# Performance work log

Hardware: AMD Instinct MI355X
Metric: run time of the kernel (lower is better)

Reference implementation:

```python
import jax, jax.numpy as jnp
import numpy as np

B, S, D_IN, D, H, HD, HALF, L = 64, 500, 64, 128, 8, 16, 5, 2
WIN = 2 * HALF + 1  # 11 attended positions per query
EPS = 1e-12  # HF layer_norm_eps default


def _ln(x, g, b):
    m = x.mean(-1, keepdims=True)
    v = ((x - m) ** 2).mean(-1, keepdims=True)
    return (x - m) / jnp.sqrt(v + EPS) * g + b


def setup_inputs() -> dict:
    key = jax.random.key(0)
    ks = jax.random.split(key, 24)
    n = lambda i, shape: jax.random.normal(ks[i], shape, jnp.float32) * 0.02
    return {
        "x": jax.random.normal(ks[0], (B, S, D_IN), jnp.float32),
        "W_in": n(1, (D_IN, D)), "b_in": jnp.zeros((D,), jnp.float32),
        "pos_emb": n(2, (512, D)), "tt_emb": n(3, (D,)),
        "ln_emb_g": jnp.ones((D,), jnp.float32), "ln_emb_b": jnp.zeros((D,), jnp.float32),
        "Wq": n(4, (L, D, D)), "bq": jnp.zeros((L, D), jnp.float32),
        "Wk": n(5, (L, D, D)), "bk": jnp.zeros((L, D), jnp.float32),
        "Wv": n(6, (L, D, D)), "bv": jnp.zeros((L, D), jnp.float32),
        "Wo": n(7, (L, D, D)), "bo": jnp.zeros((L, D), jnp.float32),
        "ln1_g": jnp.ones((L, D), jnp.float32), "ln1_b": jnp.zeros((L, D), jnp.float32),
        "Wi": n(8, (L, D, 512)), "bi": jnp.zeros((L, 512), jnp.float32),
        "Wo2": n(9, (L, 512, D)), "bo2": jnp.zeros((L, D), jnp.float32),
        "ln2_g": jnp.ones((L, D), jnp.float32), "ln2_b": jnp.zeros((L, D), jnp.float32),
        "W_cls": n(10, (D, 2)), "b_cls": jnp.zeros((2,), jnp.float32),
    }


def reference(x, W_in, b_in, pos_emb, tt_emb, ln_emb_g, ln_emb_b,
              Wq, bq, Wk, bk, Wv, bv, Wo, bo, ln1_g, ln1_b,
              Wi, bi, Wo2, bo2, ln2_g, ln2_b, W_cls, b_cls):
    # input projection + RoBERTa-style embeddings (position ids start at padding_idx+1=2)
    h = x @ W_in + b_in
    pos_ids = 2 + jnp.arange(S)
    h = _ln(h + pos_emb[pos_ids] + tt_emb, ln_emb_g, ln_emb_b)

    # sliding-window gather indices: each query attends [i-HALF, i+HALF]
    idx = jnp.arange(S)[:, None] + jnp.arange(-HALF, HALF + 1)[None, :]
    valid = (idx >= 0) & (idx < S)
    idxc = jnp.clip(idx, 0, S - 1)
    scale = 1.0 / jnp.sqrt(jnp.float32(HD))

    for l in range(L):
        qh = (h @ Wq[l] + bq[l]).reshape(B, S, H, HD).transpose(0, 2, 1, 3)
        kh = (h @ Wk[l] + bk[l]).reshape(B, S, H, HD).transpose(0, 2, 1, 3)
        vh = (h @ Wv[l] + bv[l]).reshape(B, S, H, HD).transpose(0, 2, 1, 3)
        kk = kh[:, :, idxc]
        scores = jnp.einsum('bhsd,bhswd->bhsw', qh * scale, kk)
        scores = jnp.where(valid, scores, -jnp.inf)
        probs = jax.nn.softmax(scores, axis=-1)
        vv = vh[:, :, idxc]
        ctx = jnp.einsum('bhsw,bhswd->bhsd', probs, vv)
        ctx = ctx.transpose(0, 2, 1, 3).reshape(B, S, D)
        h = _ln(ctx @ Wo[l] + bo[l] + h, ln1_g[l], ln1_b[l])
        ff = jax.nn.gelu(h @ Wi[l] + bi[l], approximate=False) @ Wo2[l] + bo2[l]
        h = _ln(ff + h, ln2_g[l], ln2_b[l])

    pooled = h.mean(axis=1)  # mean over sequence
    return pooled @ W_cls + b_cls
```

## Files before the change

### kernel.cpp

```cpp
#include <hip/hip_runtime.h>
#include <hip/hip_bf16.h>
#include <math.h>

#define BB 64
#define SS 500
#define DIN 64
#define DD 128
#define HH 8
#define HDIM 16
#define HALF_ 5
#define WINW 11
#define LL 2
#define FF 512
#define MM (BB*SS)
#define LN_EPS 1e-12f

typedef __attribute__((ext_vector_type(8))) short short8;
typedef __attribute__((ext_vector_type(4))) float f32x4;

__global__ __launch_bounds__(256) void k_prep(
    const float* __restrict__ Wq, const float* __restrict__ Wk,
    const float* __restrict__ Wv, const float* __restrict__ Wo,
    const float* __restrict__ Wi, const float* __restrict__ Wo2,
    __hip_bfloat16* __restrict__ wT)
{
    const int m = blockIdx.y;
    const int l = m / 6, t = m % 6;
    const float* src; int Kd, Nd, kshift, doff;
    switch (t) {
      case 0:  src = Wq  + l*16384; Kd=128; Nd=128; kshift=7; doff=0;      break;
      case 1:  src = Wk  + l*16384; Kd=128; Nd=128; kshift=7; doff=16384;  break;
      case 2:  src = Wv  + l*16384; Kd=128; Nd=128; kshift=7; doff=32768;  break;
      case 3:  src = Wo  + l*16384; Kd=128; Nd=128; kshift=7; doff=49152;  break;
      case 4:  src = Wi  + l*65536; Kd=128; Nd=512; kshift=7; doff=65536;  break;
      default: src = Wo2 + l*65536; Kd=512; Nd=128; kshift=9; doff=131072; break;
    }
    __hip_bfloat16* dst = wT + l*196608 + doff;
    const int NK = Kd * Nd;
    int e = (blockIdx.x * 256 + threadIdx.x) * 4;
    if (e >= NK) return;
    #pragma unroll
    for (int j = 0; j < 4; ++j, ++e) {
        int n = e >> kshift, kx = e & (Kd - 1);
        dst[(size_t)n * Kd + kx] = __float2bfloat16(src[(size_t)kx * Nd + n]);
    }
}

__global__ __launch_bounds__(256) void k_embed(
    const float* __restrict__ x, const float* __restrict__ Win,
    const float* __restrict__ bin, const float* __restrict__ pos,
    const float* __restrict__ tt, const float* __restrict__ g,
    const float* __restrict__ be, float* __restrict__ h,
    __hip_bfloat16* __restrict__ hbf)
{
    __shared__ float WinS[DIN][DD];
    __shared__ float xs[16][DIN];
    __shared__ float rs[4][2];

    const int tid = threadIdx.x;
    const int d    = tid & 127;
    const int rp   = tid >> 7;
    const int wid  = tid >> 6;
    const int row0 = blockIdx.x * 16;

    #pragma unroll
    for (int it = 0; it < 8; ++it) {
        int lin = it * 1024 + tid * 4;
        *(float4*)&WinS[lin >> 7][lin & 127] = *(const float4*)(Win + lin);
    }
    {
        int lin = tid * 4;
        *(float4*)&xs[lin >> 6][lin & 63] =
            *(const float4*)(x + (size_t)row0 * DIN + lin);
    }
    __syncthreads();

    const float bd = bin[d] + tt[d];

    for (int it = 0; it < 8; ++it) {
        const int r   = it * 2 + rp;
        const int row = row0 + r;
        const int s   = row % SS;

        float acc = bd + pos[(size_t)(2 + s) * DD + d];
        #pragma unroll 8
        for (int i = 0; i < DIN; ++i) acc += xs[r][i] * WinS[i][d];

        float s1 = acc, s2 = acc * acc;
        #pragma unroll
        for (int off = 1; off < 64; off <<= 1) {
            s1 += __shfl_xor(s1, off);
            s2 += __shfl_xor(s2, off);
        }
        if ((tid & 63) == 0) { rs[wid][0] = s1; rs[wid][1] = s2; }
        __syncthreads();
        const float S1 = rs[rp * 2][0] + rs[rp * 2 + 1][0];
        const float S2 = rs[rp * 2][1] + rs[rp * 2 + 1][1];
        const float mean = S1 * (1.0f / DD);
        const float var  = S2 * (1.0f / DD) - mean * mean;
        const float rstd = rsqrtf(var + LN_EPS);
        const float o = (acc - mean) * rstd * g[d] + be[d];
        h[(size_t)row * DD + d]   = o;
        hbf[(size_t)row * DD + d] = __float2bfloat16(o);
        __syncthreads();
    }
}

#define GEMM_MAIN(Abf, lda, Kdim, WTbf, ldw, n0w)                             \
    __shared__ __align__(16) __hip_bfloat16 As[128][72];                      \
    __shared__ __align__(16) __hip_bfloat16 Ws[128][72];                      \
    const int tid = threadIdx.x;                                              \
    const int wid = tid >> 6;                                                 \
    const int l15 = tid & 15;                                                 \
    const int l4  = (tid & 63) >> 4;                                          \
    const int m0  = blockIdx.x * 128;                                         \
    f32x4 acc[2][8];                                                          \
    _Pragma("unroll")                                                         \
    for (int m = 0; m < 2; ++m)                                               \
        _Pragma("unroll")                                                     \
        for (int n = 0; n < 8; ++n) acc[m][n] = (f32x4){0.f, 0.f, 0.f, 0.f};  \
    for (int k0 = 0; k0 < (Kdim); k0 += 64) {                                 \
        _Pragma("unroll")                                                     \
        for (int it = 0; it < 4; ++it) {                                      \
            int lin = it * 2048 + tid * 8;                                    \
            int r = lin >> 6, c = lin & 63;                                   \
            *(uint4*)&As[r][c] =                                              \
                *(const uint4*)((Abf) + (size_t)(m0 + r) * (lda) + k0 + c);   \
            *(uint4*)&Ws[r][c] =                                              \
                *(const uint4*)((WTbf) + (size_t)((n0w) + r) * (ldw) + k0 + c); \
        }                                                                     \
        __syncthreads();                                                      \
        for (int kc = 0; kc < 64; kc += 32) {                                 \
            short8 a0 = *(const short8*)&As[wid * 32 +      l15][kc + l4 * 8];\
            short8 a1 = *(const short8*)&As[wid * 32 + 16 + l15][kc + l4 * 8];\
            _Pragma("unroll")                                                 \
            for (int n = 0; n < 8; ++n) {                                     \
                short8 bf = *(const short8*)&Ws[n * 16 + l15][kc + l4 * 8];   \
                acc[0][n] = __builtin_amdgcn_mfma_f32_16x16x32_bf16(a0, bf, acc[0][n], 0, 0, 0); \
                acc[1][n] = __builtin_amdgcn_mfma_f32_16x16x32_bf16(a1, bf, acc[1][n], 0, 0, 0); \
            }                                                                 \
        }                                                                     \
        __syncthreads();                                                      \
    }

__global__ __launch_bounds__(256, 4) void k_gemm_qkv(
    const __hip_bfloat16* __restrict__ hbf,
    const __hip_bfloat16* __restrict__ wTq, const __hip_bfloat16* __restrict__ wTk,
    const __hip_bfloat16* __restrict__ wTv,
    const float* __restrict__ bq, const float* __restrict__ bk,
    const float* __restrict__ bv,
    float* __restrict__ q, float* __restrict__ k, float* __restrict__ v)
{
    const __hip_bfloat16* WT; const float* bias; float* out;
    if (blockIdx.y == 0)      { WT = wTq; bias = bq; out = q; }
    else if (blockIdx.y == 1) { WT = wTk; bias = bk; out = k; }
    else                      { WT = wTv; bias = bv; out = v; }
    GEMM_MAIN(hbf, DD, DD, WT, DD, 0)
    #pragma unroll
    for (int m = 0; m < 2; ++m)
        #pragma unroll
        for (int qq = 0; qq < 4; ++qq) {
            const int row = m0 + wid * 32 + m * 16 + l4 * 4 + qq;
            #pragma unroll
            for (int n = 0; n < 8; ++n) {
                const int col = n * 16 + l15;
                out[(size_t)row * DD + col] = acc[m][n][qq] + bias[col];
            }
        }
}

__global__ __launch_bounds__(256, 4) void k_gemm_gelu(
    const __hip_bfloat16* __restrict__ hbf,
    const __hip_bfloat16* __restrict__ wTi,
    const float* __restrict__ bias, __hip_bfloat16* __restrict__ hid)
{
    const int n0g = blockIdx.y * 128;
    GEMM_MAIN(hbf, DD, DD, wTi, DD, n0g)
    #pragma unroll
    for (int m = 0; m < 2; ++m)
        #pragma unroll
        for (int qq = 0; qq < 4; ++qq) {
            const int row = m0 + wid * 32 + m * 16 + l4 * 4 + qq;
            #pragma unroll
            for (int n = 0; n < 8; ++n) {
                const int col = n0g + n * 16 + l15;
                float val = acc[m][n][qq] + bias[col];
                val = 0.5f * val * (1.f + erff(val * 0.70710678118f));
                hid[(size_t)row * FF + col] = __float2bfloat16(val);
            }
        }
}

__global__ __launch_bounds__(256, 4) void k_gemm_lnres(
    const __hip_bfloat16* __restrict__ Abf, int lda, int Kdim,
    const __hip_bfloat16* __restrict__ WT,
    const float* __restrict__ bias, const float* __restrict__ res,
    const float* __restrict__ g, const float* __restrict__ bt,
    float* __restrict__ outF, __hip_bfloat16* __restrict__ outB)
{
    GEMM_MAIN(Abf, lda, Kdim, WT, Kdim, 0)
    #pragma unroll
    for (int m = 0; m < 2; ++m)
        #pragma unroll
        for (int qq = 0; qq < 4; ++qq) {
            const int row = m0 + wid * 32 + m * 16 + l4 * 4 + qq;
            float vals[8]; float s1 = 0.f, s2 = 0.f;
            #pragma unroll
            for (int n = 0; n < 8; ++n) {
                const int col = n * 16 + l15;
                float val = acc[m][n][qq] + bias[col] + res[(size_t)row * DD + col];
                vals[n] = val; s1 += val; s2 += val * val;
            }
            #pragma unroll
            for (int off = 1; off < 16; off <<= 1) {
                s1 += __shfl_xor(s1, off, 16);
                s2 += __shfl_xor(s2, off, 16);
            }
            const float mean = s1 * (1.0f / DD);
            const float var  = s2 * (1.0f / DD) - mean * mean;
            const float rstd = rsqrtf(var + LN_EPS);
            #pragma unroll
            for (int n = 0; n < 8; ++n) {
                const int col = n * 16 + l15;
                const float o = (vals[n] - mean) * rstd * g[col] + bt[col];
                outF[(size_t)row * DD + col] = o;
                outB[(size_t)row * DD + col] = __float2bfloat16(o);
            }
        }
}

__global__ __launch_bounds__(256) void k_attn(
    const float* __restrict__ q, const float* __restrict__ k,
    const float* __restrict__ v, __hip_bfloat16* __restrict__ ctx)
{
    __shared__ float kS[26][17], vS[26][17], qS[16][17], pS[16][16];

    const int tile = blockIdx.x, hh = blockIdx.y, b = blockIdx.z;
    const int s0  = tile * 16;
    const int tid = threadIdx.x;

    for (int e = tid; e < 26 * 16; e += 256) {
        const int r = e >> 4, d = e & 15;
        const int sr = s0 - 5 + r;
        const bool ok = (sr >= 0) && (sr < SS);
        const size_t src = ((size_t)(b * SS + (ok ? sr : 0))) * DD + hh * HDIM + d;
        kS[r][d] = ok ? k[src] : 0.f;
        vS[r][d] = ok ? v[src] : 0.f;
    }
    {
        const int gg = tid >> 4, d = tid & 15;
        const int sq = s0 + gg;
        qS[gg][d] = (sq < SS) ? q[((size_t)(b * SS + sq)) * DD + hh * HDIM + d] : 0.f;
    }
    __syncthreads();

    const int g = tid >> 4;
    const int w = tid & 15;
    const int sq = s0 + g;
    const int sw = sq + w - HALF_;
    const bool valid = (w < WINW) && (sw >= 0) && (sw < SS) && (sq < SS);

    float sc = 0.f;
    #pragma unroll
    for (int d = 0; d < HDIM; ++d) sc += qS[g][d] * kS[g + w][d];
    sc = valid ? sc * 0.25f : -INFINITY;

    float mx = sc;
    #pragma unroll
    for (int off = 1; off < 16; off <<= 1) mx = fmaxf(mx, __shfl_xor(mx, off, 16));
    float p = valid ? __expf(sc - mx) : 0.f;
    float den = p;
    #pragma unroll
    for (int off = 1; off < 16; off <<= 1) den += __shfl_xor(den, off, 16);
    pS[g][w] = p / den;

    float cd = 0.f;
    #pragma unroll
    for (int w2 = 0; w2 < WINW; ++w2) cd += pS[g][w2] * vS[g + w2][w];
    if (sq < SS)
        ctx[((size_t)(b * SS + sq)) * DD + hh * HDIM + w] = __float2bfloat16(cd);
}

__global__ __launch_bounds__(128) void k_final(
    const float* __restrict__ h, const float* __restrict__ Wc,
    const float* __restrict__ bc, float* __restrict__ out)
{
    const int b = blockIdx.x, d = threadIdx.x;
    float p = 0.f;
    for (int s = 0; s < SS; ++s) p += h[((size_t)(b * SS + s)) * DD + d];
    p *= (1.0f / SS);
    float l0 = p * Wc[d * 2 + 0];
    float l1 = p * Wc[d * 2 + 1];
    #pragma unroll
    for (int off = 1; off < 64; off <<= 1) {
        l0 += __shfl_xor(l0, off);
        l1 += __shfl_xor(l1, off);
    }
    __shared__ float r[2][2];
    const int wid = d >> 6;
    if ((d & 63) == 0) { r[wid][0] = l0; r[wid][1] = l1; }
    __syncthreads();
    if (d == 0) {
        out[b * 2 + 0] = r[0][0] + r[1][0] + bc[0];
        out[b * 2 + 1] = r[0][1] + r[1][1] + bc[1];
    }
}

extern "C" void kernel_launch(void* const* d_in, const int* in_sizes, int n_in,
                              void* d_out, int out_size, void* d_ws, size_t ws_size,
                              hipStream_t stream)
{
    const float* x      = (const float*)d_in[0];
    const float* W_in   = (const float*)d_in[1];
    const float* b_in   = (const float*)d_in[2];
    const float* pos    = (const float*)d_in[3];
    const float* tt     = (const float*)d_in[4];
    const float* lng    = (const float*)d_in[5];
    const float* lnb    = (const float*)d_in[6];
    const float* Wq     = (const float*)d_in[7];
    const float* bq     = (const float*)d_in[8];
    const float* Wk     = (const float*)d_in[9];
    const float* bk     = (const float*)d_in[10];
    const float* Wv     = (const float*)d_in[11];
    const float* bv     = (const float*)d_in[12];
    const float* Wo     = (const float*)d_in[13];
    const float* bo     = (const float*)d_in[14];
    const float* ln1g   = (const float*)d_in[15];
    const float* ln1b   = (const float*)d_in[16];
    const float* Wi     = (const float*)d_in[17];
    const float* bi     = (const float*)d_in[18];
    const float* Wo2    = (const float*)d_in[19];
    const float* bo2    = (const float*)d_in[20];
    const float* ln2g   = (const float*)d_in[21];
    const float* ln2b   = (const float*)d_in[22];
    const float* Wc     = (const float*)d_in[23];
    const float* bc     = (const float*)d_in[24];

    float*          ws    = (float*)d_ws;
    float*          h     = ws;
    __hip_bfloat16* hbf   = (__hip_bfloat16*)(ws + 4096000);
    __hip_bfloat16* ctxbf = (__hip_bfloat16*)(ws + 6144000);
    __hip_bfloat16* wT    = (__hip_bfloat16*)(ws + 8192000);
    float*          q     = ws + 8400000;
    float*          kk    = ws + 12496000;
    float*          vv    = ws + 16592000;
    __hip_bfloat16* hid   = (__hip_bfloat16*)q;

    k_prep<<<dim3(64, 12), 256, 0, stream>>>(Wq, Wk, Wv, Wo, Wi, Wo2, wT);
    k_embed<<<MM / 16, 256, 0, stream>>>(x, W_in, b_in, pos, tt, lng, lnb, h, hbf);

    for (int l = 0; l < LL; ++l) {
        const __hip_bfloat16* wTq  = wT + l * 196608;
        const __hip_bfloat16* wTk  = wTq + 16384;
        const __hip_bfloat16* wTv  = wTq + 32768;
        const __hip_bfloat16* wTo  = wTq + 49152;
        const __hip_bfloat16* wTi  = wTq + 65536;
        const __hip_bfloat16* wTo2 = wTq + 131072;

        k_gemm_qkv<<<dim3(MM / 128, 3), 256, 0, stream>>>(
            hbf, wTq, wTk, wTv, bq + l * DD, bk + l * DD, bv + l * DD, q, kk, vv);

        k_attn<<<dim3(32, HH, BB), 256, 0, stream>>>(q, kk, vv, ctxbf);

        k_gemm_lnres<<<dim3(MM / 128, 1), 256, 0, stream>>>(
            ctxbf, DD, DD, wTo, bo + l * DD, h, ln1g + l * DD, ln1b + l * DD, h, hbf);

        k_gemm_gelu<<<dim3(MM / 128, 4), 256, 0, stream>>>(
            hbf, wTi, bi + l * FF, hid);

        k_gemm_lnres<<<dim3(MM / 128, 1), 256, 0, stream>>>(
            hid, FF, FF, wTo2, bo2 + l * DD, h, ln2g + l * DD, ln2b + l * DD, h, hbf);
    }

    k_final<<<BB, 128, 0, stream>>>(h, Wc, bc, (float*)d_out);
}
```

Measured before the change: 386.7 us.

## Store Q/K/V in bf16 and halve GEMM row tile to 64

Q, K and V are now written as bf16 instead of fp32 and converted back to float when attention loads them. This halves the global traffic between the QKV projection and the attention kernel. Separately, the shared GEMM macro's M-tile shrinks from 128 to 64 rows, one 16-row MFMA strip per wave, which doubles the grid size to give more blocks per CU. The smaller tile lowers register and LDS use but reloads the weight tile twice as often, and bf16 Q/K/V lose some precision.

Result: no change. 392.0 us (+1.4%).

```diff
diff --git a/kernel.cpp b/kernel.cpp
--- a/kernel.cpp
+++ b/kernel.cpp
@@ -107,37 +107,39 @@
 }
 
 #define GEMM_MAIN(Abf, lda, Kdim, WTbf, ldw, n0w)                             \
-    __shared__ __align__(16) __hip_bfloat16 As[128][72];                      \
+    __shared__ __align__(16) __hip_bfloat16 As[64][72];                       \
     __shared__ __align__(16) __hip_bfloat16 Ws[128][72];                      \
     const int tid = threadIdx.x;                                              \
     const int wid = tid >> 6;                                                 \
     const int l15 = tid & 15;                                                 \
     const int l4  = (tid & 63) >> 4;                                          \
-    const int m0  = blockIdx.x * 128;                                         \
-    f32x4 acc[2][8];                                                          \
+    const int m0  = blockIdx.x * 64;                                          \
+    f32x4 acc[8];                                                             \
     _Pragma("unroll")                                                         \
-    for (int m = 0; m < 2; ++m)                                               \
+    for (int n = 0; n < 8; ++n) acc[n] = (f32x4){0.f, 0.f, 0.f, 0.f};         \
+    for (int k0 = 0; k0 < (Kdim); k0 += 64) {                                 \
         _Pragma("unroll")                                                     \
-        for (int n = 0; n < 8; ++n) acc[m][n] = (f32x4){0.f, 0.f, 0.f, 0.f};  \
-    for (int k0 = 0; k0 < (Kdim); k0 += 64) {                                 \
+        for (int it = 0; it < 2; ++it) {                                      \
+            int lin = it * 2048 + tid * 8;                                    \
+            int r = lin >> 6, c = lin & 63;                                   \
+            *(uint4*)&As[r][c] =                                              \
+                *(const uint4*)((Abf) + (size_t)(m0 + r) * (lda) + k0 + c);   \
+        }                                                                     \
         _Pragma("unroll")                                                     \
         for (int it = 0; it < 4; ++it) {                                      \
             int lin = it * 2048 + tid * 8;                                    \
             int r = lin >> 6, c = lin & 63;                                   \
-            *(uint4*)&As[r][c] =                                              \
-                *(const uint4*)((Abf) + (size_t)(m0 + r) * (lda) + k0 + c);   \
             *(uint4*)&Ws[r][c] =                                              \
                 *(const uint4*)((WTbf) + (size_t)((n0w) + r) * (ldw) + k0 + c); \
         }                                                                     \
         __syncthreads();                                                      \
+        _Pragma("unroll")                                                     \
         for (int kc = 0; kc < 64; kc += 32) {                                 \
-            short8 a0 = *(const short8*)&As[wid * 32 +      l15][kc + l4 * 8];\
-            short8 a1 = *(const short8*)&As[wid * 32 + 16 + l15][kc + l4 * 8];\
+            short8 a0 = *(const short8*)&As[wid * 16 + l15][kc + l4 * 8];     \
             _Pragma("unroll")                                                 \
             for (int n = 0; n < 8; ++n) {                                     \
                 short8 bf = *(const short8*)&Ws[n * 16 + l15][kc + l4 * 8];   \
-                acc[0][n] = __builtin_amdgcn_mfma_f32_16x16x32_bf16(a0, bf, acc[0][n], 0, 0, 0); \
-                acc[1][n] = __builtin_amdgcn_mfma_f32_16x16x32_bf16(a1, bf, acc[1][n], 0, 0, 0); \
+                acc[n] = __builtin_amdgcn_mfma_f32_16x16x32_bf16(a0, bf, acc[n], 0, 0, 0); \
             }                                                                 \
         }                                                                     \
         __syncthreads();                                                      \
@@ -149,24 +151,23 @@
     const __hip_bfloat16* __restrict__ wTv,
     const float* __restrict__ bq, const float* __restrict__ bk,
     const float* __restrict__ bv,
-    float* __restrict__ q, float* __restrict__ k, float* __restrict__ v)
-{
-    const __hip_bfloat16* WT; const float* bias; float* out;
+    __hip_bfloat16* __restrict__ q, __hip_bfloat16* __restrict__ k,
+    __hip_bfloat16* __restrict__ v)
+{
+    const __hip_bfloat16* WT; const float* bias; __hip_bfloat16* out;
     if (blockIdx.y == 0)      { WT = wTq; bias = bq; out = q; }
     else if (blockIdx.y == 1) { WT = wTk; bias = bk; out = k; }
     else                      { WT = wTv; bias = bv; out = v; }
     GEMM_MAIN(hbf, DD, DD, WT, DD, 0)
     #pragma unroll
-    for (int m = 0; m < 2; ++m)
-        #pragma unroll
-        for (int qq = 0; qq < 4; ++qq) {
-            const int row = m0 + wid * 32 + m * 16 + l4 * 4 + qq;
-            #pragma unroll
-            for (int n = 0; n < 8; ++n) {
-                const int col = n * 16 + l15;
-                out[(size_t)row * DD + col] = acc[m][n][qq] + bias[col];
-            }
-        }
+    for (int qq = 0; qq < 4; ++qq) {
+        const int row = m0 + wid * 16 + l4 * 4 + qq;
+        #pragma unroll
+        for (int n = 0; n < 8; ++n) {
+            const int col = n * 16 + l15;
+            out[(size_t)row * DD + col] = __float2bfloat16(acc[n][qq] + bias[col]);
+        }
+    }
 }
 
 __global__ __launch_bounds__(256, 4) void k_gemm_gelu(
@@ -177,18 +178,16 @@
     const int n0g = blockIdx.y * 128;
     GEMM_MAIN(hbf, DD, DD, wTi, DD, n0g)
     #pragma unroll
-    for (int m = 0; m < 2; ++m)
-        #pragma unroll
-        for (int qq = 0; qq < 4; ++qq) {
-            const int row = m0 + wid * 32 + m * 16 + l4 * 4 + qq;
-            #pragma unroll
-            for (int n = 0; n < 8; ++n) {
-                const int col = n0g + n * 16 + l15;
-                float val = acc[m][n][qq] + bias[col];
-                val = 0.5f * val * (1.f + erff(val * 0.70710678118f));
-                hid[(size_t)row * FF + col] = __float2bfloat16(val);
-            }
-        }
+    for (int qq = 0; qq < 4; ++qq) {
+        const int row = m0 + wid * 16 + l4 * 4 + qq;
+        #pragma unroll
+        for (int n = 0; n < 8; ++n) {
+            const int col = n0g + n * 16 + l15;
+            float val = acc[n][qq] + bias[col];
+            val = 0.5f * val * (1.f + erff(val * 0.70710678118f));
+            hid[(size_t)row * FF + col] = __float2bfloat16(val);
+        }
+    }
 }
 
 __global__ __launch_bounds__(256, 4) void k_gemm_lnres(
@@ -200,38 +199,36 @@
 {
     GEMM_MAIN(Abf, lda, Kdim, WT, Kdim, 0)
     #pragma unroll
-    for (int m = 0; m < 2; ++m)
-        #pragma unroll
-        for (int qq = 0; qq < 4; ++qq) {
-            const int row = m0 + wid * 32 + m * 16 + l4 * 4 + qq;
-            float vals[8]; float s1 = 0.f, s2 = 0.f;
-            #pragma unroll
-            for (int n = 0; n < 8; ++n) {
-                const int col = n * 16 + l15;
-                float val = acc[m][n][qq] + bias[col] + res[(size_t)row * DD + col];
-                vals[n] = val; s1 += val; s2 += val * val;
-            }
-            #pragma unroll
-            for (int off = 1; off < 16; off <<= 1) {
-                s1 += __shfl_xor(s1, off, 16);
-                s2 += __shfl_xor(s2, off, 16);
-            }
-            const float mean = s1 * (1.0f / DD);
-            const float var  = s2 * (1.0f / DD) - mean * mean;
-            const float rstd = rsqrtf(var + LN_EPS);
-            #pragma unroll
-            for (int n = 0; n < 8; ++n) {
-                const int col = n * 16 + l15;
-                const float o = (vals[n] - mean) * rstd * g[col] + bt[col];
-                outF[(size_t)row * DD + col] = o;
-                outB[(size_t)row * DD + col] = __float2bfloat16(o);
-            }
-        }
+    for (int qq = 0; qq < 4; ++qq) {
+        const int row = m0 + wid * 16 + l4 * 4 + qq;
+        float vals[8]; float s1 = 0.f, s2 = 0.f;
+        #pragma unroll
+        for (int n = 0; n < 8; ++n) {
+            const int col = n * 16 + l15;
+            float val = acc[n][qq] + bias[col] + res[(size_t)row * DD + col];
+            vals[n] = val; s1 += val; s2 += val * val;
+        }
+        #pragma unroll
+        for (int off = 1; off < 16; off <<= 1) {
+            s1 += __shfl_xor(s1, off, 16);
+            s2 += __shfl_xor(s2, off, 16);
+        }
+        const float mean = s1 * (1.0f / DD);
+        const float var  = s2 * (1.0f / DD) - mean * mean;
+        const float rstd = rsqrtf(var + LN_EPS);
+        #pragma unroll
+        for (int n = 0; n < 8; ++n) {
+            const int col = n * 16 + l15;
+            const float o = (vals[n] - mean) * rstd * g[col] + bt[col];
+            outF[(size_t)row * DD + col] = o;
+            outB[(size_t)row * DD + col] = __float2bfloat16(o);
+        }
+    }
 }
 
 __global__ __launch_bounds__(256) void k_attn(
-    const float* __restrict__ q, const float* __restrict__ k,
-    const float* __restrict__ v, __hip_bfloat16* __restrict__ ctx)
+    const __hip_bfloat16* __restrict__ q, const __hip_bfloat16* __restrict__ k,
+    const __hip_bfloat16* __restrict__ v, __hip_bfloat16* __restrict__ ctx)
 {
     __shared__ float kS[26][17], vS[26][17], qS[16][17], pS[16][16];
 
@@ -244,13 +241,14 @@
         const int sr = s0 - 5 + r;
         const bool ok = (sr >= 0) && (sr < SS);
         const size_t src = ((size_t)(b * SS + (ok ? sr : 0))) * DD + hh * HDIM + d;
-        kS[r][d] = ok ? k[src] : 0.f;
-        vS[r][d] = ok ? v[src] : 0.f;
+        kS[r][d] = ok ? __bfloat162float(k[src]) : 0.f;
+        vS[r][d] = ok ? __bfloat162float(v[src]) : 0.f;
     }
     {
         const int gg = tid >> 4, d = tid & 15;
         const int sq = s0 + gg;
-        qS[gg][d] = (sq < SS) ? q[((size_t)(b * SS + sq)) * DD + hh * HDIM + d] : 0.f;
+        qS[gg][d] = (sq < SS)
+            ? __bfloat162float(q[((size_t)(b * SS + sq)) * DD + hh * HDIM + d]) : 0.f;
     }
     __syncthreads();
 
@@ -341,10 +339,10 @@
     __hip_bfloat16* hbf   = (__hip_bfloat16*)(ws + 4096000);
     __hip_bfloat16* ctxbf = (__hip_bfloat16*)(ws + 6144000);
     __hip_bfloat16* wT    = (__hip_bfloat16*)(ws + 8192000);
-    float*          q     = ws + 8400000;
-    float*          kk    = ws + 12496000;
-    float*          vv    = ws + 16592000;
-    __hip_bfloat16* hid   = (__hip_bfloat16*)q;
+    __hip_bfloat16* q     = (__hip_bfloat16*)(ws + 8400000);
+    __hip_bfloat16* kk    = (__hip_bfloat16*)(ws + 10448000);
+    __hip_bfloat16* vv    = (__hip_bfloat16*)(ws + 12496000);
+    __hip_bfloat16* hid   = q;
 
     k_prep<<<dim3(64, 12), 256, 0, stream>>>(Wq, Wk, Wv, Wo, Wi, Wo2, wT);
     k_embed<<<MM / 16, 256, 0, stream>>>(x, W_in, b_in, pos, tt, lng, lnb, h, hbf);
@@ -357,18 +355,18 @@
         const __hip_bfloat16* wTi  = wTq + 65536;
         const __hip_bfloat16* wTo2 = wTq + 131072;
 
-        k_gemm_qkv<<<dim3(MM / 128, 3), 256, 0, stream>>>(
+        k_gemm_qkv<<<dim3(MM / 64, 3), 256, 0, stream>>>(
             hbf, wTq, wTk, wTv, bq + l * DD, bk + l * DD, bv + l * DD, q, kk, vv);
 
         k_attn<<<dim3(32, HH, BB), 256, 0, stream>>>(q, kk, vv, ctxbf);
 
-        k_gemm_lnres<<<dim3(MM / 128, 1), 256, 0, stream>>>(
+        k_gemm_lnres<<<dim3(MM / 64, 1), 256, 0, stream>>>(
             ctxbf, DD, DD, wTo, bo + l * DD, h, ln1g + l * DD, ln1b + l * DD, h, hbf);
 
-        k_gemm_gelu<<<dim3(MM / 128, 4), 256, 0, stream>>>(
+        k_gemm_gelu<<<dim3(MM / 64, 4), 256, 0, stream>>>(
             hbf, wTi, bi + l * FF, hid);
 
-        k_gemm_lnres<<<dim3(MM / 128, 1), 256, 0, stream>>>(
+        k_gemm_lnres<<<dim3(MM / 64, 1), 256, 0, stream>>>(
             hid, FF, FF, wTo2, bo2 + l * DD, h, ln2g + l * DD, ln2b + l * DD, h, hbf);
     }
 
```
